# Optimization experiments

Measured on AMD Instinct MI355X. Metric: run time of the kernel, lower is better.

## Reference

```python
import jax, jax.numpy as jnp
import numpy as np

B, S, E, H = 2, 2048, 768, 12
D = E // H  # head_dim = 64
SCALE = D ** -0.5
NEG = float(np.finfo(np.float32).max)


def setup_inputs() -> dict:
    key = jax.random.key(0)
    ks = jax.random.split(key, 6)
    std = E ** -0.5
    return {
        "inputs": jax.random.normal(ks[0], (B, S, E), dtype=jnp.float32),
        "mask": jax.random.randint(ks[1], (B, S), 0, 2, dtype=jnp.int32),
        "w_qkv": jax.random.normal(ks[2], (3 * E, E), dtype=jnp.float32) * std,
        "b_qkv": jax.random.normal(ks[3], (3 * E,), dtype=jnp.float32) * 0.01,
        "w_proj": jax.random.normal(ks[4], (E, E), dtype=jnp.float32) * std,
        "b_proj": jax.random.normal(ks[5], (E,), dtype=jnp.float32) * 0.01,
    }


def reference(inputs, mask, w_qkv, b_qkv, w_proj, b_proj):
    # qkv projection: (B,S,E) -> (B,S,3E) -> (3,B,H,S,D)
    qkv = (jnp.einsum("bse,fe->bsf", inputs, w_qkv) + b_qkv)
    qkv = qkv.reshape(B, S, 3, H, D).transpose(2, 0, 3, 1, 4)
    q, k, v = qkv[0], qkv[1], qkv[2]
    # scaled dot-product scores (B,H,S,S)
    qk = jnp.einsum("bhqd,bhkd->bhqk", q, k) * SCALE
    # mask (B,S) broadcasts over key axis, matching torch broadcasting
    qk = qk + mask.astype(jnp.float32)[:, None, None, :] * (-NEG)
    attn = jax.nn.softmax(qk, axis=-1)
    x = jnp.einsum("bhqk,bhkd->bhqd", attn, v)  # (B,H,S,D)
    x = x.transpose(0, 2, 1, 3).reshape(B, S, E)
    # dropouts are identity in eval mode
    return jnp.einsum("bse,fe->bsf", x, w_proj) + b_proj
```

## Files before the change

kernel.cpp:

```cpp
#include <hip/hip_runtime.h>
#include <stdint.h>

#define S_LEN 2048
#define EMB   768
#define NHEAD 12
#define HDIM  64

typedef __attribute__((ext_vector_type(8)))  __bf16       bf16x8;
typedef __attribute__((ext_vector_type(4)))  float        f32x4;
typedef __attribute__((ext_vector_type(16))) float        f32x16;
typedef __attribute__((ext_vector_type(2)))  unsigned int u32x2;
typedef __attribute__((ext_vector_type(4)))  unsigned int u32x4;

__device__ __forceinline__ uint16_t f32_to_bf16(float f) {
  uint32_t u = __float_as_uint(f);
  u += 0x7FFFu + ((u >> 16) & 1u);
  return (uint16_t)(u >> 16);
}

__device__ __forceinline__ uint32_t cvtpk_bf16(float lo, float hi) {
  uint32_t r;
  asm("v_cvt_pk_bf16_f32 %0, %1, %2" : "=v"(r) : "v"(lo), "v"(hi));
  return r;
}

#if __has_builtin(__builtin_amdgcn_exp2f)
#define EXP2F(x) __builtin_amdgcn_exp2f(x)
#else
#define EXP2F(x) exp2f(x)
#endif

#define ZERO16 {0.f,0.f,0.f,0.f,0.f,0.f,0.f,0.f,0.f,0.f,0.f,0.f,0.f,0.f,0.f,0.f}

__device__ __forceinline__ int swz64(int idx) {
  return idx ^ (((idx >> 6) & 7) << 3);
}

__device__ __forceinline__ void gload16(uint16_t* lds, const uint16_t* g) {
  __builtin_amdgcn_global_load_lds((const __attribute__((address_space(1))) void*)g,
                                   (__attribute__((address_space(3))) void*)lds, 16, 0, 0);
}

__global__ __launch_bounds__(256) void cvt_all(const float4* __restrict__ i0, ushort4* __restrict__ o0, int n0,
                                               const float4* __restrict__ i1, ushort4* __restrict__ o1, int n1,
                                               const float4* __restrict__ i2, ushort4* __restrict__ o2, int n2) {
  int gid = blockIdx.x * blockDim.x + threadIdx.x;
  const float4* src;
  ushort4* dst;
  int idx;
  if (gid < n0)           { src = i0; dst = o0; idx = gid; }
  else if (gid < n0 + n1) { src = i1; dst = o1; idx = gid - n0; }
  else if (gid < n0 + n1 + n2) { src = i2; dst = o2; idx = gid - n0 - n1; }
  else return;
  float4 v = src[idx];
  ushort4 o;
  o.x = f32_to_bf16(v.x); o.y = f32_to_bf16(v.y);
  o.z = f32_to_bf16(v.z); o.w = f32_to_bf16(v.w);
  dst[idx] = o;
}

__global__ __launch_bounds__(256) void mask_scan(const int* __restrict__ mask,
                                                 int* __restrict__ cpos,
                                                 float* __restrict__ mbc,
                                                 int* __restrict__ ntp,
                                                 int* __restrict__ nbp) {
  const int b    = blockIdx.x;
  const int t    = threadIdx.x;
  const int lane = t & 63;
  const int wvi  = t >> 6;
  __shared__ int wsum[4];
  int m[8], u = 0;
#pragma unroll
  for (int j = 0; j < 8; j++) {
    m[j] = mask[b * S_LEN + t * 8 + j];
    u += (m[j] == 0);
  }
  int x = u;
#pragma unroll
  for (int off = 1; off < 64; off <<= 1) {
    int v = __shfl_up(x, off);
    if (lane >= off) x += v;
  }
  if (lane == 63) wsum[wvi] = x;
  __syncthreads();
  int wbase = 0;
#pragma unroll
  for (int i = 0; i < 4; i++) wbase += (i < wvi) ? wsum[i] : 0;
  const int nb = wsum[0] + wsum[1] + wsum[2] + wsum[3];
  int base = wbase + x - u;
#pragma unroll
  for (int j = 0; j < 8; j++) {
    int sc = (m[j] == 0) ? base : -1;
    if (m[j] == 0) base++;
    cpos[b * S_LEN + t * 8 + j] = sc;
    mbc[b * S_LEN + t * 8 + j] = ((t * 8 + j) < nb) ? 0.0f : -1e30f;
  }
  if (t == 0) {
    ntp[b] = ((nb + 63) & ~63) >> 6;
    nbp[b] = nb;
  }
}

__global__ __launch_bounds__(256) void pad_fill(const int* __restrict__ nbp,
                                                uint16_t* __restrict__ kb,
                                                uint16_t* __restrict__ vb) {
  const int b = blockIdx.x / NHEAD, h = blockIdx.x % NHEAD;
  const int t = threadIdx.x;
  const int nb = nbp[b];
  const int padN = (nb + 63) & ~63;
  const int npad = padN - nb;
  for (int idx = t; idx < npad * HDIM; idx += 256) {
    int row = idx >> 6, d = idx & (HDIM - 1);
    kb[(((size_t)b * NHEAD + h) * S_LEN + nb + row) * HDIM + d] = 0;
    vb[(((size_t)b * NHEAD + h) * HDIM + d) * S_LEN + nb + row] = 0;
  }
}

__global__ __launch_bounds__(256) void qkv_gemm(const uint16_t* __restrict__ A,
                                                const uint16_t* __restrict__ W,
                                                const float* __restrict__ bias,
                                                const int* __restrict__ cpos,
                                                uint16_t* __restrict__ qb,
                                                uint16_t* __restrict__ kb,
                                                uint16_t* __restrict__ vb) {
  __shared__ __align__(16) uint16_t As[128 * 64];
  __shared__ __align__(16) uint16_t Bs[64 * 64];
  const int t    = threadIdx.x;
  const int lane = t & 63;
  const int wv   = t >> 6;
  const int wr   = wv >> 1, wc = wv & 1;
  const int wg   = (blockIdx.x & 7) * 144 + (blockIdx.x >> 3);
  const int bm   = wg / 36;
  const int bn   = wg % 36;

  const uint16_t* Ag = A + (size_t)bm * 128 * 768;
  const uint16_t* Wg = W + (size_t)bn * 64 * 768;

  f32x4 zf = {0.f, 0.f, 0.f, 0.f};
  f32x4 acc[4][2];
#pragma unroll
  for (int m = 0; m < 4; m++)
#pragma unroll
    for (int n = 0; n < 2; n++) acc[m][n] = zf;

  for (int k0 = 0; k0 < 768; k0 += 64) {
#pragma unroll
    for (int j = 0; j < 4; j++) {
      int p = j * 256 + t;
      int r = p >> 3, x = p & 7;
      int scol = (x ^ (r & 7)) << 3;
      gload16(&As[p * 8], Ag + (size_t)r * 768 + k0 + scol);
    }
#pragma unroll
    for (int j = 0; j < 2; j++) {
      int p = j * 256 + t;
      int r = p >> 3, x = p & 7;
      int scol = (x ^ (r & 7)) << 3;
      gload16(&Bs[p * 8], Wg + (size_t)r * 768 + k0 + scol);
    }
    __syncthreads();
#pragma unroll
    for (int kk = 0; kk < 2; kk++) {
      const int kc = kk * 32 + (lane >> 4) * 8;
      bf16x8 af[4], bf[2];
#pragma unroll
      for (int m = 0; m < 4; m++)
        af[m] = *reinterpret_cast<const bf16x8*>(&As[swz64((wr * 64 + m * 16 + (lane & 15)) * 64 + kc)]);
#pragma unroll
      for (int n = 0; n < 2; n++)
        bf[n] = *reinterpret_cast<const bf16x8*>(&Bs[swz64((wc * 32 + n * 16 + (lane & 15)) * 64 + kc)]);
#pragma unroll
      for (int m = 0; m < 4; m++)
#pragma unroll
        for (int n = 0; n < 2; n++)
          acc[m][n] = __builtin_amdgcn_mfma_f32_16x16x32_bf16(af[m], bf[n], acc[m][n], 0, 0, 0);
    }
    __syncthreads();
  }

  const int cQ = bn / 12;
  int scv[4][4];
  if (cQ != 0) {
#pragma unroll
    for (int m = 0; m < 4; m++)
#pragma unroll
      for (int r = 0; r < 4; r++) {
        int i = bm * 128 + wr * 64 + m * 16 + (lane >> 4) * 4 + r;
        scv[m][r] = cpos[(i >> 11) * S_LEN + (i & 2047)];
      }
  }
#pragma unroll
  for (int n = 0; n < 2; n++) {
    const int f   = bn * 64 + wc * 32 + n * 16 + (lane & 15);
    const float bv = bias[f];
    const int rem = f - cQ * 768;
    const int h   = rem >> 6, d = rem & 63;
    const float scl = (cQ == 0) ? 0.125f * 1.44269504f : 1.0f;
#pragma unroll
    for (int m = 0; m < 4; m++) {
#pragma unroll
      for (int r = 0; r < 4; r++) {
        int i = bm * 128 + wr * 64 + m * 16 + (lane >> 4) * 4 + r;
        int b = i >> 11, s = i & 2047;
        uint16_t val = f32_to_bf16((acc[m][n][r] + bv) * scl);
        if (cQ == 0) {
          qb[(((size_t)b * NHEAD + h) * S_LEN + s) * HDIM + d] = val;
        } else {
          int sc = scv[m][r];
          if (sc >= 0) {
            if (cQ == 1)
              kb[(((size_t)b * NHEAD + h) * S_LEN + sc) * HDIM + d] = val;
            else
              vb[(((size_t)b * NHEAD + h) * HDIM + d) * S_LEN + sc] = val;
          }
        }
      }
    }
  }
}

__global__ __launch_bounds__(256, 3) void attn_kernel(const uint16_t* __restrict__ Q,
                                                      const uint16_t* __restrict__ Kb,
                                                      const uint16_t* __restrict__ Vb,
                                                      const float* __restrict__ mbc,
                                                      const int* __restrict__ ntp,
                                                      uint16_t* __restrict__ X) {
  __shared__ __align__(16) uint16_t Kd[2][64 * 64];
  __shared__ __align__(16) uint16_t Vd[2][64 * 64];
  __shared__ __align__(16) float    mb_s[S_LEN];
  __shared__ float Lc[2][32];

  const int t    = threadIdx.x;
  const int lane = t & 63;
  const int hl   = lane >> 5;
  const int q31  = lane & 31;
  const int wv   = t >> 6;
  const int qg   = wv & 1;
  const int kh   = wv >> 1;
  const int wg   = (blockIdx.x & 7) * 96 + (blockIdx.x >> 3);
  const int qblk = wg & 31;
  const int bh   = wg >> 5;
  const int b    = bh / NHEAD, hd = bh % NHEAD;

  const uint16_t* Qh = Q  + (size_t)bh * S_LEN * HDIM;
  const uint16_t* Kh = Kb + (size_t)bh * S_LEN * HDIM;
  const uint16_t* Vh = Vb + (size_t)bh * HDIM * S_LEN;
  const int q0 = qblk * 64 + qg * 32;
  const int nt = ntp[b];

  {
    float4 f0 = *reinterpret_cast<const float4*>(&mbc[b * S_LEN + t * 8]);
    float4 f1 = *reinterpret_cast<const float4*>(&mbc[b * S_LEN + t * 8 + 4]);
    *reinterpret_cast<float4*>(&mb_s[t * 8])     = f0;
    *reinterpret_cast<float4*>(&mb_s[t * 8 + 4]) = f1;
  }

  bf16x8 qf[4];
#pragma unroll
  for (int s = 0; s < 4; s++)
    qf[s] = *reinterpret_cast<const bf16x8*>(Qh + (size_t)(q0 + q31) * HDIM + 16 * s + 8 * hl);

  f32x16 oacc[2] = {ZERO16, ZERO16};
  float lsum = 0.f;

  const uint16_t* kga[2]; const uint16_t* vga[2]; int lof[2];
#pragma unroll
  for (int j = 0; j < 2; j++) {
    int p = j * 256 + t, r = p >> 3, x = p & 7;
    int scol = (x ^ (r & 7)) << 3;
    kga[j] = Kh + (size_t)r * HDIM + scol;
    vga[j] = Vh + (size_t)r * S_LEN + scol;
    lof[j] = p * 8;
  }
  auto stage = [&](int nb2, int it2) {
#pragma unroll
    for (int j = 0; j < 2; j++) {
      gload16(&Kd[nb2][lof[j]], kga[j] + it2 * 64 * HDIM);
      gload16(&Vd[nb2][lof[j]], vga[j] + it2 * 64);
    }
  };

  stage(0, 0);
  __syncthreads();

#pragma unroll 2
  for (int it = 0; it < nt; ++it) {
    const int cur = it & 1;
    __builtin_amdgcn_s_barrier();
    __builtin_amdgcn_sched_barrier(0);
    if (it + 1 < nt) {
      stage(cur ^ 1, it + 1);
      asm volatile("s_waitcnt vmcnt(4)" ::: "memory");
    } else {
      asm volatile("s_waitcnt vmcnt(0)" ::: "memory");
    }
    __builtin_amdgcn_s_barrier();
    __builtin_amdgcn_sched_barrier(0);

    f32x16 scc = ZERO16;
    __builtin_amdgcn_s_setprio(1);
#pragma unroll
    for (int s = 0; s < 4; s++) {
      bf16x8 kf = *reinterpret_cast<const bf16x8*>(&Kd[cur][swz64((kh * 32 + q31) * 64 + 16 * s + 8 * hl)]);
      scc = __builtin_amdgcn_mfma_f32_32x32x16_bf16(kf, qf[s], scc, 0, 0, 0);
    }
    __builtin_amdgcn_s_setprio(0);

    uint32_t w[4][2];
    if (it == nt - 1) {
#pragma unroll
      for (int s2 = 0; s2 < 4; s2++) {
        f32x4 mbv = *reinterpret_cast<const f32x4*>(&mb_s[it * 64 + kh * 32 + s2 * 8 + hl * 4]);
        float p0 = EXP2F(scc[4 * s2 + 0] + mbv[0]);
        float p1 = EXP2F(scc[4 * s2 + 1] + mbv[1]);
        float p2 = EXP2F(scc[4 * s2 + 2] + mbv[2]);
        float p3 = EXP2F(scc[4 * s2 + 3] + mbv[3]);
        lsum += (p0 + p1) + (p2 + p3);
        w[s2][0] = cvtpk_bf16(p0, p1);
        w[s2][1] = cvtpk_bf16(p2, p3);
      }
    } else {
#pragma unroll
      for (int s2 = 0; s2 < 4; s2++) {
        float p0 = EXP2F(scc[4 * s2 + 0]);
        float p1 = EXP2F(scc[4 * s2 + 1]);
        float p2 = EXP2F(scc[4 * s2 + 2]);
        float p3 = EXP2F(scc[4 * s2 + 3]);
        lsum += (p0 + p1) + (p2 + p3);
        w[s2][0] = cvtpk_bf16(p0, p1);
        w[s2][1] = cvtpk_bf16(p2, p3);
      }
    }

    bf16x8 pb[2];
#pragma unroll
    for (int ks = 0; ks < 2; ks++) {
      u32x2 r0 = __builtin_amdgcn_permlane32_swap(w[2 * ks][0], w[2 * ks + 1][0], false, false);
      u32x2 r1 = __builtin_amdgcn_permlane32_swap(w[2 * ks][1], w[2 * ks + 1][1], false, false);
      u32x4 uu;
      uu.x = r0.x; uu.y = r1.x; uu.z = r0.y; uu.w = r1.y;
      pb[ks] = __builtin_bit_cast(bf16x8, uu);
    }

    __builtin_amdgcn_s_setprio(1);
#pragma unroll
    for (int mt = 0; mt < 2; mt++)
#pragma unroll
      for (int ks = 0; ks < 2; ks++) {
        bf16x8 vf = *reinterpret_cast<const bf16x8*>(&Vd[cur][swz64((mt * 32 + q31) * 64 + kh * 32 + ks * 16 + hl * 8)]);
        oacc[mt] = __builtin_amdgcn_mfma_f32_32x32x16_bf16(vf, pb[ks], oacc[mt], 0, 0, 0);
      }
    __builtin_amdgcn_s_setprio(0);
  }

  lsum += __shfl_xor(lsum, 32);

  __syncthreads();

  float* Oc = qg ? (float*)&Vd[0][0] : (float*)&Kd[0][0];
  if (kh == 1) {
#pragma unroll
    for (int mt = 0; mt < 2; mt++)
#pragma unroll
      for (int e = 0; e < 16; e++) {
        int d = mt * 32 + (e & 3) + (e >> 2) * 8 + hl * 4;
        Oc[d * 32 + q31] = oacc[mt][e];
      }
    if (hl == 0) Lc[qg][q31] = lsum;
  }
  __syncthreads();
  if (kh == 0) {
    float linv = 1.0f / (lsum + Lc[qg][q31]);
    uint16_t* Xr = X + ((size_t)b * S_LEN + q0 + q31) * EMB + hd * HDIM;
#pragma unroll
    for (int mt = 0; mt < 2; mt++)
#pragma unroll
      for (int s2 = 0; s2 < 4; s2++) {
        int d0 = mt * 32 + s2 * 8 + hl * 4;
        float v0 = (oacc[mt][4 * s2 + 0] + Oc[(d0 + 0) * 32 + q31]) * linv;
        float v1 = (oacc[mt][4 * s2 + 1] + Oc[(d0 + 1) * 32 + q31]) * linv;
        float v2 = (oacc[mt][4 * s2 + 2] + Oc[(d0 + 2) * 32 + q31]) * linv;
        float v3 = (oacc[mt][4 * s2 + 3] + Oc[(d0 + 3) * 32 + q31]) * linv;
        uint2 ww;
        ww.x = cvtpk_bf16(v0, v1);
        ww.y = cvtpk_bf16(v2, v3);
        *reinterpret_cast<uint2*>(Xr + d0) = ww;
      }
  }
}

__global__ __launch_bounds__(256) void proj_gemm(const uint16_t* __restrict__ A,
                                                 const uint16_t* __restrict__ W,
                                                 const float* __restrict__ bias,
                                                 float* __restrict__ out) {
  __shared__ __align__(16) uint16_t As[64 * 64];
  __shared__ __align__(16) uint16_t Bs[64 * 64];
  const int t    = threadIdx.x;
  const int lane = t & 63;
  const int wv   = t >> 6;
  const int wr   = wv >> 1, wc = wv & 1;
  const int wg   = (blockIdx.x & 7) * 96 + (blockIdx.x >> 3);
  const int bm   = wg / 12;
  const int bn   = wg % 12;

  const uint16_t* Ag = A + (size_t)bm * 64 * 768;
  const uint16_t* Wg = W + (size_t)bn * 64 * 768;

  f32x4 zf = {0.f, 0.f, 0.f, 0.f};
  f32x4 acc[2][2];
#pragma unroll
  for (int m = 0; m < 2; m++)
#pragma unroll
    for (int n = 0; n < 2; n++) acc[m][n] = zf;

  for (int k0 = 0; k0 < 768; k0 += 64) {
#pragma unroll
    for (int j = 0; j < 2; j++) {
      int p = j * 256 + t;
      int r = p >> 3, x = p & 7;
      int scol = (x ^ (r & 7)) << 3;
      gload16(&As[p * 8], Ag + (size_t)r * 768 + k0 + scol);
      gload16(&Bs[p * 8], Wg + (size_t)r * 768 + k0 + scol);
    }
    __syncthreads();
#pragma unroll
    for (int kk = 0; kk < 2; kk++) {
      const int kc = kk * 32 + (lane >> 4) * 8;
      bf16x8 af[2], bf[2];
#pragma unroll
      for (int m = 0; m < 2; m++)
        af[m] = *reinterpret_cast<const bf16x8*>(&As[swz64((wr * 32 + m * 16 + (lane & 15)) * 64 + kc)]);
#pragma unroll
      for (int n = 0; n < 2; n++)
        bf[n] = *reinterpret_cast<const bf16x8*>(&Bs[swz64((wc * 32 + n * 16 + (lane & 15)) * 64 + kc)]);
#pragma unroll
      for (int m = 0; m < 2; m++)
#pragma unroll
        for (int n = 0; n < 2; n++)
          acc[m][n] = __builtin_amdgcn_mfma_f32_16x16x32_bf16(af[m], bf[n], acc[m][n], 0, 0, 0);
    }
    __syncthreads();
  }

#pragma unroll
  for (int n = 0; n < 2; n++) {
    const int f = bn * 64 + wc * 32 + n * 16 + (lane & 15);
    const float bv = bias[f];
#pragma unroll
    for (int m = 0; m < 2; m++)
#pragma unroll
      for (int r = 0; r < 4; r++) {
        int i = bm * 64 + wr * 32 + m * 16 + (lane >> 4) * 4 + r;
        out[(size_t)i * 768 + f] = acc[m][n][r] + bv;
      }
  }
}

extern "C" void kernel_launch(void* const* d_in, const int* in_sizes, int n_in,
                              void* d_out, int out_size, void* d_ws, size_t ws_size,
                              hipStream_t stream) {
  const float* inputs = (const float*)d_in[0];
  const int*   mask   = (const int*)d_in[1];
  const float* w_qkv  = (const float*)d_in[2];
  const float* b_qkv  = (const float*)d_in[3];
  const float* w_proj = (const float*)d_in[4];
  const float* b_proj = (const float*)d_in[5];
  float* out = (float*)d_out;

  uint16_t* a_bf  = (uint16_t*)d_ws;
  uint16_t* wq_bf = a_bf  + (size_t)4096 * 768;
  uint16_t* wp_bf = wq_bf + (size_t)2304 * 768;
  uint16_t* q_bf  = wp_bf + (size_t)768 * 768;
  uint16_t* k_bf  = q_bf  + (size_t)24 * 2048 * 64;
  uint16_t* v_bf  = k_bf  + (size_t)24 * 2048 * 64;
  uint16_t* x_bf  = v_bf  + (size_t)24 * 2048 * 64;
  int*      cpos  = (int*)(x_bf + (size_t)4096 * 768);
  float*    mbc   = (float*)(cpos + 2 * 2048);
  int*      ntp   = (int*)(mbc + 2 * 2048);
  int*      nbp   = ntp + 2;

  const int n0 = 4096 * 768 / 4, n1 = 2304 * 768 / 4, n2 = 768 * 768 / 4;
  cvt_all<<<(n0 + n1 + n2 + 255) / 256, 256, 0, stream>>>(
      (const float4*)inputs, (ushort4*)a_bf, n0,
      (const float4*)w_qkv,  (ushort4*)wq_bf, n1,
      (const float4*)w_proj, (ushort4*)wp_bf, n2);
  mask_scan<<<2, 256, 0, stream>>>(mask, cpos, mbc, ntp, nbp);
  pad_fill<<<2 * NHEAD, 256, 0, stream>>>(nbp, k_bf, v_bf);
  qkv_gemm<<<32 * 36, 256, 0, stream>>>(a_bf, wq_bf, b_qkv, cpos, q_bf, k_bf, v_bf);
  attn_kernel<<<24 * 32, 256, 0, stream>>>(q_bf, k_bf, v_bf, mbc, ntp, x_bf);
  proj_gemm<<<64 * 12, 256, 0, stream>>>(x_bf, wp_bf, b_proj, out);
}
```

Before: 83.11 us.

## Gather unmasked input rows before QKV GEMM and skip fully masked K/V tiles

```diff
diff --git a/kernel.cpp b/kernel.cpp
--- a/kernel.cpp
+++ b/kernel.cpp
@@ -11,6 +11,7 @@
 typedef __attribute__((ext_vector_type(16))) float        f32x16;
 typedef __attribute__((ext_vector_type(2)))  unsigned int u32x2;
 typedef __attribute__((ext_vector_type(4)))  unsigned int u32x4;
+typedef __attribute__((ext_vector_type(8)))  uint16_t     u16x8;
 
 __device__ __forceinline__ uint16_t f32_to_bf16(float f) {
   uint32_t u = __float_as_uint(f);
@@ -60,7 +61,7 @@
 }
 
 __global__ __launch_bounds__(256) void mask_scan(const int* __restrict__ mask,
-                                                 int* __restrict__ cpos,
+                                                 int* __restrict__ gpos,
                                                  float* __restrict__ mbc,
                                                  int* __restrict__ ntp,
                                                  int* __restrict__ nbp) {
@@ -90,9 +91,10 @@
   int base = wbase + x - u;
 #pragma unroll
   for (int j = 0; j < 8; j++) {
-    int sc = (m[j] == 0) ? base : -1;
-    if (m[j] == 0) base++;
-    cpos[b * S_LEN + t * 8 + j] = sc;
+    if (m[j] == 0) {
+      gpos[b * S_LEN + base] = t * 8 + j;
+      base++;
+    }
     mbc[b * S_LEN + t * 8 + j] = ((t * 8 + j) < nb) ? 0.0f : -1e30f;
   }
   if (t == 0) {
@@ -101,25 +103,35 @@
   }
 }
 
-__global__ __launch_bounds__(256) void pad_fill(const int* __restrict__ nbp,
-                                                uint16_t* __restrict__ kb,
-                                                uint16_t* __restrict__ vb) {
-  const int b = blockIdx.x / NHEAD, h = blockIdx.x % NHEAD;
-  const int t = threadIdx.x;
-  const int nb = nbp[b];
-  const int padN = (nb + 63) & ~63;
-  const int npad = padN - nb;
-  for (int idx = t; idx < npad * HDIM; idx += 256) {
-    int row = idx >> 6, d = idx & (HDIM - 1);
-    kb[(((size_t)b * NHEAD + h) * S_LEN + nb + row) * HDIM + d] = 0;
-    vb[(((size_t)b * NHEAD + h) * HDIM + d) * S_LEN + nb + row] = 0;
+__global__ __launch_bounds__(256) void gather_kv(const uint16_t* __restrict__ a,
+                                                 const int* __restrict__ gpos,
+                                                 const int* __restrict__ nbp,
+                                                 uint16_t* __restrict__ akv) {
+  const int t   = threadIdx.x;
+  const int row = blockIdx.x * 16 + (t >> 4);
+  const int b   = row >> 11, i = row & 2047;
+  const int nb  = nbp[b];
+  const int c16 = (t & 15) * 48;
+  uint16_t* dp = akv + (size_t)row * 768 + c16;
+  if (i >= nb) {
+    u16x8 z = {0, 0, 0, 0, 0, 0, 0, 0};
+#pragma unroll
+    for (int j = 0; j < 6; j++)
+      *reinterpret_cast<u16x8*>(dp + j * 8) = z;
+  } else {
+    const int s = gpos[b * S_LEN + i];
+    const uint16_t* sp = a + ((size_t)b * S_LEN + s) * 768 + c16;
+#pragma unroll
+    for (int j = 0; j < 6; j++)
+      *reinterpret_cast<u16x8*>(dp + j * 8) = *reinterpret_cast<const u16x8*>(sp + j * 8);
   }
 }
 
 __global__ __launch_bounds__(256) void qkv_gemm(const uint16_t* __restrict__ A,
+                                                const uint16_t* __restrict__ Akv,
                                                 const uint16_t* __restrict__ W,
                                                 const float* __restrict__ bias,
-                                                const int* __restrict__ cpos,
+                                                const int* __restrict__ nbp,
                                                 uint16_t* __restrict__ qb,
                                                 uint16_t* __restrict__ kb,
                                                 uint16_t* __restrict__ vb) {
@@ -132,8 +144,16 @@
   const int wg   = (blockIdx.x & 7) * 144 + (blockIdx.x >> 3);
   const int bm   = wg / 36;
   const int bn   = wg % 36;
-
-  const uint16_t* Ag = A + (size_t)bm * 128 * 768;
+  const int cQ   = bn / 12;
+
+  if (cQ != 0) {
+    const int batch = bm >> 4;
+    const int l0    = (bm & 15) * 128;
+    const int padN  = (nbp[batch] + 63) & ~63;
+    if (l0 >= padN) return;
+  }
+
+  const uint16_t* Ag = (cQ == 0 ? A : Akv) + (size_t)bm * 128 * 768;
   const uint16_t* Wg = W + (size_t)bn * 64 * 768;
 
   f32x4 zf = {0.f, 0.f, 0.f, 0.f};
@@ -178,17 +198,6 @@
     __syncthreads();
   }
 
-  const int cQ = bn / 12;
-  int scv[4][4];
-  if (cQ != 0) {
-#pragma unroll
-    for (int m = 0; m < 4; m++)
-#pragma unroll
-      for (int r = 0; r < 4; r++) {
-        int i = bm * 128 + wr * 64 + m * 16 + (lane >> 4) * 4 + r;
-        scv[m][r] = cpos[(i >> 11) * S_LEN + (i & 2047)];
-      }
-  }
 #pragma unroll
   for (int n = 0; n < 2; n++) {
     const int f   = bn * 64 + wc * 32 + n * 16 + (lane & 15);
@@ -203,17 +212,12 @@
         int i = bm * 128 + wr * 64 + m * 16 + (lane >> 4) * 4 + r;
         int b = i >> 11, s = i & 2047;
         uint16_t val = f32_to_bf16((acc[m][n][r] + bv) * scl);
-        if (cQ == 0) {
+        if (cQ == 0)
           qb[(((size_t)b * NHEAD + h) * S_LEN + s) * HDIM + d] = val;
-        } else {
-          int sc = scv[m][r];
-          if (sc >= 0) {
-            if (cQ == 1)
-              kb[(((size_t)b * NHEAD + h) * S_LEN + sc) * HDIM + d] = val;
-            else
-              vb[(((size_t)b * NHEAD + h) * HDIM + d) * S_LEN + sc] = val;
-          }
-        }
+        else if (cQ == 1)
+          kb[(((size_t)b * NHEAD + h) * S_LEN + s) * HDIM + d] = val;
+        else
+          vb[(((size_t)b * NHEAD + h) * HDIM + d) * S_LEN + s] = val;
       }
     }
   }
@@ -474,8 +478,9 @@
   uint16_t* k_bf  = q_bf  + (size_t)24 * 2048 * 64;
   uint16_t* v_bf  = k_bf  + (size_t)24 * 2048 * 64;
   uint16_t* x_bf  = v_bf  + (size_t)24 * 2048 * 64;
-  int*      cpos  = (int*)(x_bf + (size_t)4096 * 768);
-  float*    mbc   = (float*)(cpos + 2 * 2048);
+  uint16_t* akv   = x_bf  + (size_t)4096 * 768;
+  int*      gpos  = (int*)(akv + (size_t)4096 * 768);
+  float*    mbc   = (float*)(gpos + 2 * 2048);
   int*      ntp   = (int*)(mbc + 2 * 2048);
   int*      nbp   = ntp + 2;
 
@@ -484,9 +489,9 @@
       (const float4*)inputs, (ushort4*)a_bf, n0,
       (const float4*)w_qkv,  (ushort4*)wq_bf, n1,
       (const float4*)w_proj, (ushort4*)wp_bf, n2);
-  mask_scan<<<2, 256, 0, stream>>>(mask, cpos, mbc, ntp, nbp);
-  pad_fill<<<2 * NHEAD, 256, 0, stream>>>(nbp, k_bf, v_bf);
-  qkv_gemm<<<32 * 36, 256, 0, stream>>>(a_bf, wq_bf, b_qkv, cpos, q_bf, k_bf, v_bf);
+  mask_scan<<<2, 256, 0, stream>>>(mask, gpos, mbc, ntp, nbp);
+  gather_kv<<<256, 256, 0, stream>>>(a_bf, gpos, nbp, akv);
+  qkv_gemm<<<32 * 36, 256, 0, stream>>>(a_bf, akv, wq_bf, b_qkv, nbp, q_bf, k_bf, v_bf);
   attn_kernel<<<24 * 32, 256, 0, stream>>>(q_bf, k_bf, v_bf, mbc, ntp, x_bf);
   proj_gemm<<<64 * 12, 256, 0, stream>>>(x_bf, wp_bf, b_proj, out);
 }
```

After: 87.94 us. +5.8%, slower.

## Widen QKV GEMM tiles to three N-subtiles per block for A reuse

Applied to the files above, without the earlier changes.

```diff
diff --git a/kernel.cpp b/kernel.cpp
--- a/kernel.cpp
+++ b/kernel.cpp
@@ -124,24 +124,27 @@
                                                 uint16_t* __restrict__ kb,
                                                 uint16_t* __restrict__ vb) {
   __shared__ __align__(16) uint16_t As[128 * 64];
-  __shared__ __align__(16) uint16_t Bs[64 * 64];
+  __shared__ __align__(16) uint16_t Bs[3][64 * 64];
   const int t    = threadIdx.x;
   const int lane = t & 63;
   const int wv   = t >> 6;
   const int wr   = wv >> 1, wc = wv & 1;
-  const int wg   = (blockIdx.x & 7) * 144 + (blockIdx.x >> 3);
-  const int bm   = wg / 36;
-  const int bn   = wg % 36;
+  const int wg   = (blockIdx.x & 7) * 48 + (blockIdx.x >> 3);
+  const int bm   = wg / 12;
+  const int bng  = wg % 12;
+  const int cQ   = bng >> 2;
 
   const uint16_t* Ag = A + (size_t)bm * 128 * 768;
-  const uint16_t* Wg = W + (size_t)bn * 64 * 768;
+  const uint16_t* Wg = W + (size_t)(bng * 3) * 64 * 768;
 
   f32x4 zf = {0.f, 0.f, 0.f, 0.f};
-  f32x4 acc[4][2];
-#pragma unroll
-  for (int m = 0; m < 4; m++)
-#pragma unroll
-    for (int n = 0; n < 2; n++) acc[m][n] = zf;
+  f32x4 acc[3][4][2];
+#pragma unroll
+  for (int g = 0; g < 3; g++)
+#pragma unroll
+    for (int m = 0; m < 4; m++)
+#pragma unroll
+      for (int n = 0; n < 2; n++) acc[g][m][n] = zf;
 
   for (int k0 = 0; k0 < 768; k0 += 64) {
 #pragma unroll
@@ -152,33 +155,38 @@
       gload16(&As[p * 8], Ag + (size_t)r * 768 + k0 + scol);
     }
 #pragma unroll
-    for (int j = 0; j < 2; j++) {
-      int p = j * 256 + t;
-      int r = p >> 3, x = p & 7;
-      int scol = (x ^ (r & 7)) << 3;
-      gload16(&Bs[p * 8], Wg + (size_t)r * 768 + k0 + scol);
-    }
+    for (int g = 0; g < 3; g++)
+#pragma unroll
+      for (int j = 0; j < 2; j++) {
+        int p = j * 256 + t;
+        int r = p >> 3, x = p & 7;
+        int scol = (x ^ (r & 7)) << 3;
+        gload16(&Bs[g][p * 8], Wg + (size_t)(g * 64 + r) * 768 + k0 + scol);
+      }
     __syncthreads();
 #pragma unroll
     for (int kk = 0; kk < 2; kk++) {
       const int kc = kk * 32 + (lane >> 4) * 8;
-      bf16x8 af[4], bf[2];
+      bf16x8 af[4];
 #pragma unroll
       for (int m = 0; m < 4; m++)
         af[m] = *reinterpret_cast<const bf16x8*>(&As[swz64((wr * 64 + m * 16 + (lane & 15)) * 64 + kc)]);
 #pragma unroll
-      for (int n = 0; n < 2; n++)
-        bf[n] = *reinterpret_cast<const bf16x8*>(&Bs[swz64((wc * 32 + n * 16 + (lane & 15)) * 64 + kc)]);
-#pragma unroll
-      for (int m = 0; m < 4; m++)
+      for (int g = 0; g < 3; g++) {
+        bf16x8 bf[2];
 #pragma unroll
         for (int n = 0; n < 2; n++)
-          acc[m][n] = __builtin_amdgcn_mfma_f32_16x16x32_bf16(af[m], bf[n], acc[m][n], 0, 0, 0);
+          bf[n] = *reinterpret_cast<const bf16x8*>(&Bs[g][swz64((wc * 32 + n * 16 + (lane & 15)) * 64 + kc)]);
+#pragma unroll
+        for (int m = 0; m < 4; m++)
+#pragma unroll
+          for (int n = 0; n < 2; n++)
+            acc[g][m][n] = __builtin_amdgcn_mfma_f32_16x16x32_bf16(af[m], bf[n], acc[g][m][n], 0, 0, 0);
+      }
     }
     __syncthreads();
   }
 
-  const int cQ = bn / 12;
   int scv[4][4];
   if (cQ != 0) {
 #pragma unroll
@@ -190,28 +198,31 @@
       }
   }
 #pragma unroll
-  for (int n = 0; n < 2; n++) {
-    const int f   = bn * 64 + wc * 32 + n * 16 + (lane & 15);
-    const float bv = bias[f];
-    const int rem = f - cQ * 768;
-    const int h   = rem >> 6, d = rem & 63;
-    const float scl = (cQ == 0) ? 0.125f * 1.44269504f : 1.0f;
-#pragma unroll
-    for (int m = 0; m < 4; m++) {
-#pragma unroll
-      for (int r = 0; r < 4; r++) {
-        int i = bm * 128 + wr * 64 + m * 16 + (lane >> 4) * 4 + r;
-        int b = i >> 11, s = i & 2047;
-        uint16_t val = f32_to_bf16((acc[m][n][r] + bv) * scl);
-        if (cQ == 0) {
-          qb[(((size_t)b * NHEAD + h) * S_LEN + s) * HDIM + d] = val;
-        } else {
-          int sc = scv[m][r];
-          if (sc >= 0) {
-            if (cQ == 1)
-              kb[(((size_t)b * NHEAD + h) * S_LEN + sc) * HDIM + d] = val;
-            else
-              vb[(((size_t)b * NHEAD + h) * HDIM + d) * S_LEN + sc] = val;
+  for (int g = 0; g < 3; g++) {
+#pragma unroll
+    for (int n = 0; n < 2; n++) {
+      const int f   = (bng * 3 + g) * 64 + wc * 32 + n * 16 + (lane & 15);
+      const float bv = bias[f];
+      const int rem = f - cQ * 768;
+      const int h   = rem >> 6, d = rem & 63;
+      const float scl = (cQ == 0) ? 0.125f * 1.44269504f : 1.0f;
+#pragma unroll
+      for (int m = 0; m < 4; m++) {
+#pragma unroll
+        for (int r = 0; r < 4; r++) {
+          int i = bm * 128 + wr * 64 + m * 16 + (lane >> 4) * 4 + r;
+          int b = i >> 11, s = i & 2047;
+          uint16_t val = f32_to_bf16((acc[g][m][n][r] + bv) * scl);
+          if (cQ == 0) {
+            qb[(((size_t)b * NHEAD + h) * S_LEN + s) * HDIM + d] = val;
+          } else {
+            int sc = scv[m][r];
+            if (sc >= 0) {
+              if (cQ == 1)
+                kb[(((size_t)b * NHEAD + h) * S_LEN + sc) * HDIM + d] = val;
+              else
+                vb[(((size_t)b * NHEAD + h) * HDIM + d) * S_LEN + sc] = val;
+            }
           }
         }
       }
@@ -486,7 +497,7 @@
       (const float4*)w_proj, (ushort4*)wp_bf, n2);
   mask_scan<<<2, 256, 0, stream>>>(mask, cpos, mbc, ntp, nbp);
   pad_fill<<<2 * NHEAD, 256, 0, stream>>>(nbp, k_bf, v_bf);
-  qkv_gemm<<<32 * 36, 256, 0, stream>>>(a_bf, wq_bf, b_qkv, cpos, q_bf, k_bf, v_bf);
+  qkv_gemm<<<32 * 12, 256, 0, stream>>>(a_bf, wq_bf, b_qkv, cpos, q_bf, k_bf, v_bf);
   attn_kernel<<<24 * 32, 256, 0, stream>>>(q_bf, k_bf, v_bf, mbc, ntp, x_bf);
   proj_gemm<<<64 * 12, 256, 0, stream>>>(x_bf, wp_bf, b_proj, out);
 }
```

Result: slower. 98.94 us (+19.0%).
